# Optimization experiments

Measured on AMD Instinct MI355X. Metric: run time of the kernel, lower is better.

The kernel has to match this reference:

```python
import jax, jax.numpy as jnp
import numpy as np

EPSILON = 1e-06
MAXIMUM_AREA_RATIO = 0.3
GRID_HEIGHT = 160.0
CUBE = (25.0, 25.0, 32.0)
FEAT_SCALE = 1.0
GRID_SCALE = 1.0
CRANGE = (-1.0, 0.95)


def setup_inputs() -> dict:
    key = jax.random.key(0)
    k1, k2, k3, k4, k5 = jax.random.split(key, 5)
    B, C, H, W = 2, 256, 96, 320
    L, Wg = 128, 128
    n_layers = int(GRID_HEIGHT // CUBE[2])  # 5
    return {
        "feature": jax.random.normal(k1, (B, C, H, W), dtype=jnp.float32),
        "calib": jax.random.normal(k2, (B, 3, 4), dtype=jnp.float32),
        "grid": jax.random.normal(k3, (L, Wg, 3), dtype=jnp.float32),
        "Wc": jax.random.normal(k4, (C, C * n_layers), dtype=jnp.float32) * 0.02,
        "bc": jax.random.normal(k5, (C,), dtype=jnp.float32) * 0.02,
    }


def _cube_corners(cube):
    l, w, h = cube
    x = np.array([-l / 2, l / 2, l / 2, -l / 2, -l / 2, l / 2, l / 2, -l / 2])
    y = np.array([-w / 2, -w / 2, w / 2, w / 2, -w / 2, -w / 2, w / 2, w / 2])
    z = np.array([0, 0, 0, 0, h, h, h, h])
    return jnp.asarray(np.stack([x, y, z], axis=-1), dtype=jnp.float32)  # (8,3)


def _grid_sample_zeros(img, grd):
    # img: [B,C,H,W]; grd: [B,Hg,Wg,2] normalized coords in [-1,1]
    # bilinear, zero padding, align_corners=False (torch default)
    B, C, H, W = img.shape
    x = ((grd[..., 0] + 1.0) * W - 1.0) * 0.5
    y = ((grd[..., 1] + 1.0) * H - 1.0) * 0.5
    x0f = jnp.floor(x)
    y0f = jnp.floor(y)
    x0 = x0f.astype(jnp.int32)
    y0 = y0f.astype(jnp.int32)
    img_flat = img.reshape(B, C, H * W)

    def gather(xi, yi):
        valid = (xi >= 0) & (xi < W) & (yi >= 0) & (yi < H)
        xc = jnp.clip(xi, 0, W - 1)
        yc = jnp.clip(yi, 0, H - 1)
        idx = (yc * W + xc).reshape(B, 1, -1)
        v = jnp.take_along_axis(img_flat, idx, axis=2)
        v = v.reshape((B, C) + grd.shape[1:-1])
        return v * valid[:, None].astype(img.dtype)

    wx1 = x - x0f
    wx0 = 1.0 - wx1
    wy1 = y - y0f
    wy0 = 1.0 - wy1
    out = (gather(x0, y0) * (wx0 * wy0)[:, None]
           + gather(x0 + 1, y0) * (wx1 * wy0)[:, None]
           + gather(x0, y0 + 1) * (wx0 * wy1)[:, None]
           + gather(x0 + 1, y0 + 1) * (wx1 * wy1)[:, None])
    return out


def reference(feature, calib, grid, Wc, bc):
    B, C, H, W = feature.shape
    L, Wg, _ = grid.shape
    dtype = feature.dtype

    # z-layer offsets: (n_layers, 3) with offset only in z
    z_off = jnp.arange(0.0, GRID_HEIGHT, CUBE[2], dtype=dtype)  # (5,)
    n_layers = z_off.shape[0]
    z_corners = jnp.stack([jnp.zeros_like(z_off), jnp.zeros_like(z_off), z_off], axis=-1)
    offset = _cube_corners(CUBE)  # (8,3)

    # corners3d: (n_layers, L, Wg, 8, 3)
    corners = grid[None] + z_corners[:, None, None, :]  # (n,L,Wg,3)
    corners3d = (corners[:, :, :, None, :] + offset[None, None, None]) / GRID_SCALE

    # project with calib (B,3,4): homogeneous matmul then perspective divide
    hom = jnp.concatenate([corners3d, jnp.ones_like(corners3d[..., :1])], axis=-1)  # (n,L,Wg,8,4)
    pts = jnp.einsum('bij,nlwkj->bnlwki', calib, hom)  # (B,n,L,Wg,8,3)
    img_xy = pts[..., :2] / jnp.maximum(pts[..., 2:3], EPSILON)

    img_size = jnp.array([W, H], dtype=dtype) / FEAT_SCALE
    norm = jnp.clip(2.0 * img_xy / img_size - 1.0, CRANGE[0], CRANGE[1])  # (B,n,L,Wg,8,2)

    box_corners = jnp.concatenate([
        jnp.min(norm[..., 0], axis=-1, keepdims=True),
        jnp.min(norm[..., 1], axis=-1, keepdims=True),
        jnp.max(norm[..., 0], axis=-1, keepdims=True),
        jnp.max(norm[..., 1], axis=-1, keepdims=True),
    ], axis=-1)  # (B,n,L,Wg,4)
    box_corners = box_corners.reshape(B, n_layers, L * Wg, 4)

    area = ((box_corners[..., 2:] - box_corners[..., :2]).prod(axis=-1) * (H * W) + EPSILON)
    area = area[:, None]  # (B,1,n,LWg)
    visible = ((area > EPSILON) & (area < H * W * MAXIMUM_AREA_RATIO)).astype(dtype)

    integral = jnp.cumsum(jnp.cumsum(feature, axis=-1), axis=-2)

    lt = _grid_sample_zeros(integral, box_corners[..., [0, 1]])
    rb = _grid_sample_zeros(integral, box_corners[..., [2, 3]])
    rt = _grid_sample_zeros(integral, box_corners[..., [2, 1]])
    lb = _grid_sample_zeros(integral, box_corners[..., [0, 3]])

    vox = (lt + rb - rt - lb) / area * visible  # (B,C,n,LWg)
    # permute(0,3,1,2) -> (B, LWg, C, n); flatten to (B*LWg, C*n)
    vox = jnp.transpose(vox, (0, 3, 1, 2)).reshape(B * L * Wg, C * n_layers)

    ortho = vox @ Wc.T + bc  # (B*LWg, C)
    ortho = ortho.reshape(B, L, Wg, C)
    ortho = jax.nn.relu(jnp.transpose(ortho, (0, 3, 1, 2)))  # (B,C,L,Wg)
    return ortho
```

## Files before the change

kernel.cpp:

```cpp
#include <hip/hip_runtime.h>
#include <hip/hip_bf16.h>
#include <stdint.h>

#define BB 2
#define CC 256
#define HH 96
#define WW 320
#define NPIX 16384
#define NLAY 5
#define KDIM 1280
#define NDIM 32768
#define NKT (KDIM / 32)
#define NGRP 256

typedef float f32x4 __attribute__((ext_vector_type(4)));
typedef float f32x2 __attribute__((ext_vector_type(2)));
typedef __bf16 bf16x8 __attribute__((ext_vector_type(8)));
typedef __bf16 bf16x4 __attribute__((ext_vector_type(4)));


__global__ __launch_bounds__(1024) void k1f(const float* __restrict__ feat,
                                            float* __restrict__ integ,
                                            const float* __restrict__ gridp,
                                            const float* __restrict__ calib,
                                            const float* __restrict__ Wc,
                                            float4* __restrict__ coords,
                                            float* __restrict__ scales,
                                            __bf16* __restrict__ Wbf,
                                            uint8_t* __restrict__ mask8) {
  const int bid = blockIdx.x;
  if (bid < 480) {
    const int vbid = bid * 4 + (threadIdx.x >> 8);
    const int vt = threadIdx.x & 255;
    if (vbid >= 640) {
      int o = (vbid - 640) * 256 + vt;
      int co = o / KDIM;
      int kk = o % KDIM;
      int n = kk >> 8;
      int c = kk & 255;
      Wbf[o] = (__bf16)Wc[co * KDIM + c * NLAY + n];
      return;
    }
    int box = vbid * 256 + vt;
    int pix = box & (NPIX - 1);
    int bn = box >> 14;
    int n = bn % NLAY;
    int b = bn / NLAY;
    const float* cb = calib + b * 12;
    float c00 = cb[0], c01 = cb[1], c02 = cb[2], c03 = cb[3];
    float c10 = cb[4], c11 = cb[5], c12 = cb[6], c13 = cb[7];
    float c20 = cb[8], c21 = cb[9], c22 = cb[10], c23 = cb[11];
    float gx = gridp[pix * 3 + 0], gy = gridp[pix * 3 + 1], gz = gridp[pix * 3 + 2];
    float zoff = 32.0f * (float)n;
    const float ox[8] = {-12.5f, 12.5f, 12.5f, -12.5f, -12.5f, 12.5f, 12.5f, -12.5f};
    const float oy[8] = {-12.5f, -12.5f, 12.5f, 12.5f, -12.5f, -12.5f, 12.5f, 12.5f};
    float xmn = 1e30f, ymn = 1e30f, xmx = -1e30f, ymx = -1e30f;
#pragma unroll
    for (int k = 0; k < 8; ++k) {
      float X = gx + ox[k];
      float Y = gy + oy[k];
      float Z = gz + zoff + ((k >= 4) ? 32.0f : 0.0f);
      float px = c00 * X + c01 * Y + c02 * Z + c03;
      float py = c10 * X + c11 * Y + c12 * Z + c13;
      float pz = c20 * X + c21 * Y + c22 * Z + c23;
      float d = fmaxf(pz, 1e-6f);
      float nx = fminf(fmaxf(2.0f * (px / d) / 320.0f - 1.0f, -1.0f), 0.95f);
      float ny = fminf(fmaxf(2.0f * (py / d) / 96.0f - 1.0f, -1.0f), 0.95f);
      xmn = fminf(xmn, nx); xmx = fmaxf(xmx, nx);
      ymn = fminf(ymn, ny); ymx = fmaxf(ymx, ny);
    }
    float dx = xmx - xmn, dy = ymx - ymn;
    float area = (dx * dy) * 30720.0f + 1e-6f;
    bool vis = (area > 1e-6f) && (area < 9216.0f);
    {
      __shared__ uint32_t kf[16];
      unsigned long long bal = __ballot(vis);
      if ((threadIdx.x & 63) == 0) kf[threadIdx.x >> 6] = (bal != 0ull) ? 1u : 0u;
      __syncthreads();
      if (vt == 0) {
        int vb = threadIdx.x >> 8;
        int vbid2 = bid * 4 + vb;
        int bn2 = vbid2 >> 6;
        int n2 = bn2 % NLAY, b2 = bn2 / NLAY;
        int g0 = b2 * 128 + (vbid2 & 63) * 2;
        mask8[g0 * 5 + n2]       = (uint8_t)(kf[vb * 4 + 0] | kf[vb * 4 + 1]);
        mask8[(g0 + 1) * 5 + n2] = (uint8_t)(kf[vb * 4 + 2] | kf[vb * 4 + 3]);
      }
    }
    float X0 = ((xmn + 1.0f) * 320.0f - 1.0f) * 0.5f;
    float Y0 = ((ymn + 1.0f) * 96.0f - 1.0f) * 0.5f;
    float X1 = ((xmx + 1.0f) * 320.0f - 1.0f) * 0.5f;
    float Y1 = ((ymx + 1.0f) * 96.0f - 1.0f) * 0.5f;
    coords[box] = make_float4(X0, Y0, X1, Y1);
    scales[box] = vis ? 1.0f / area : 0.0f;
    return;
  }
  __shared__ float tile[WW * 33];
  const int t = threadIdx.x;
  const int wave = t >> 6;
  const int lane = t & 63;
  const int kb = bid - 480;
  const int cg = kb & 7;
  const int h = (kb >> 3) % HH;
  const int b = kb / (8 * HH);
  const int c0 = cg * 32 + wave * 2;
  const float* s0 = feat + (size_t)((b * CC + c0) * HH + h) * WW;
  const float* s1 = s0 + (size_t)HH * WW;

  float va[5], vb[5];
#pragma unroll
  for (int j = 0; j < 5; ++j) va[j] = s0[lane * 5 + j];
#pragma unroll
  for (int j = 0; j < 5; ++j) vb[j] = s1[lane * 5 + j];
#pragma unroll
  for (int j = 1; j < 5; ++j) { va[j] += va[j - 1]; vb[j] += vb[j - 1]; }
  float ta = va[4], tb = vb[4];
  float ia = ta, ib = tb;
#pragma unroll
  for (int d = 1; d < 64; d <<= 1) {
    float ua = __shfl_up(ia, d, 64);
    float ub = __shfl_up(ib, d, 64);
    if (lane >= d) { ia += ua; ib += ub; }
  }
  float pa = ia - ta, pb = ib - tb;
#pragma unroll
  for (int j = 0; j < 5; ++j) { va[j] += pa; vb[j] += pb; }
  const int ca = wave * 2, cbn = wave * 2 + 1;
#pragma unroll
  for (int j = 0; j < 5; ++j) {
    int w = lane * 5 + j;
    tile[w * 33 + ca]  = va[j];
    tile[w * 33 + cbn] = vb[j];
  }
  __syncthreads();
  float* dst = integ + ((size_t)(b * WW) * HH + h) * CC + cg * 32;
  const size_t wstride = (size_t)HH * CC;
#pragma unroll
  for (int r = 0; r < 3; ++r) {
    int idx = r * 1024 + t;
    if (idx < 2560) {
      int w = idx >> 3;
      int cq = (idx & 7) * 4;
      float4 o = make_float4(tile[w * 33 + cq + 0], tile[w * 33 + cq + 1],
                             tile[w * 33 + cq + 2], tile[w * 33 + cq + 3]);
      *(float4*)(dst + (size_t)w * wstride + cq) = o;
    }
  }
}

__global__ __launch_bounds__(256) void k2_scan(float* __restrict__ integ) {
  const int blk = blockIdx.x;
  const int w = blk % WW;
  const int b = blk / WW;
  const int g = threadIdx.x >> 6;
  const int l = threadIdx.x & 63;
  float* base = integ + ((size_t)(b * WW + w) * HH + g * 24) * CC + l * 4;
  const size_t stride = (size_t)CC;
  f32x4 v[24];
#pragma unroll
  for (int i = 0; i < 24; ++i) v[i] = *(const f32x4*)(base + (size_t)i * stride);
#pragma unroll
  for (int i = 1; i < 24; ++i) v[i] += v[i - 1];
  __shared__ f32x4 part[4][64];
  part[g][l] = v[23];
  __syncthreads();
  f32x4 off = {0.f, 0.f, 0.f, 0.f};
#pragma unroll
  for (int gg = 0; gg < 3; ++gg)
    if (gg < g) off += part[gg][l];
#pragma unroll
  for (int i = 0; i < 24; ++i) *(f32x4*)(base + (size_t)i * stride) = v[i] + off;
}

__global__ __launch_bounds__(256) void k4_vox(const float* __restrict__ integ,
                                              const float4* __restrict__ coords,
                                              const float* __restrict__ scales,
                                              __bf16* __restrict__ voxA,
                                              const uint8_t* __restrict__ mask8) {
  const int wave = threadIdx.x >> 6;
  const int lane = threadIdx.x & 63;
  const int box0 = (blockIdx.x * 4 + wave) * 4;
  {
    const int pix0 = box0 & (NPIX - 1);
    const int bn0 = box0 >> 14;
    const int n0 = bn0 % NLAY, b0 = bn0 / NLAY;
    if (mask8[((b0 * NPIX + pix0) >> 7) * 5 + n0] == 0) return;
  }
#pragma unroll
  for (int u = 0; u < 4; ++u) {
    const int box = box0 + u;
    const int pix = box & (NPIX - 1);
    const int bn = box >> 14;
    const int n = bn % NLAY;
    const int b = bn / NLAY;
    const size_t row = (size_t)(b * NPIX + pix);
    bf16x4* dst = (bf16x4*)(voxA + row * KDIM + n * CC + lane * 4);
    const float scale = scales[box];
    if (scale == 0.f) {
      *dst = bf16x4{(__bf16)0.f, (__bf16)0.f, (__bf16)0.f, (__bf16)0.f};
      continue;
    }
    const float4 q = coords[box];

    float xw[4]; int xi[4];
    float yw[4]; int yi[4];
    {
      float f0 = floorf(q.x); int i0 = (int)f0; float w1 = q.x - f0;
      xw[0] = (i0 >= 0 && i0 < WW) ? (1.f - w1) : 0.f;
      xw[1] = (i0 + 1 < WW) ? w1 : 0.f;
      xi[0] = min(max(i0, 0), WW - 1); xi[1] = min(max(i0 + 1, 0), WW - 1);
      float f1 = floorf(q.z); int i1 = (int)f1; float v1 = q.z - f1;
      xw[2] = (i1 >= 0 && i1 < WW) ? -(1.f - v1) : 0.f;
      xw[3] = (i1 + 1 < WW) ? -v1 : 0.f;
      xi[2] = min(max(i1, 0), WW - 1); xi[3] = min(max(i1 + 1, 0), WW - 1);
    }
    {
      float f0 = floorf(q.y); int j0 = (int)f0; float w1 = q.y - f0;
      yw[0] = (j0 >= 0 && j0 < HH) ? (1.f - w1) : 0.f;
      yw[1] = (j0 + 1 < HH) ? w1 : 0.f;
      yi[0] = min(max(j0, 0), HH - 1); yi[1] = min(max(j0 + 1, 0), HH - 1);
      float f1 = floorf(q.w); int j1 = (int)f1; float v1 = q.w - f1;
      yw[2] = (j1 >= 0 && j1 < HH) ? -(1.f - v1) : 0.f;
      yw[3] = (j1 + 1 < HH) ? -v1 : 0.f;
      yi[2] = min(max(j1, 0), HH - 1); yi[3] = min(max(j1 + 1, 0), HH - 1);
    }
    const float* base = integ + (size_t)(b * WW) * HH * CC + lane * 4;
    f32x4 val = {0.f, 0.f, 0.f, 0.f};
#pragma unroll
    for (int jj = 0; jj < 4; ++jj) {
      if (yw[jj] == 0.f) continue;
      const float* rp = base + (size_t)yi[jj] * CC;
      f32x4 rs = {0.f, 0.f, 0.f, 0.f};
#pragma unroll
      for (int ii = 0; ii < 4; ++ii) {
        if (xw[ii] != 0.f) {
          f32x4 v = *(const f32x4*)(rp + (size_t)xi[ii] * HH * CC);
          rs += xw[ii] * v;
        }
      }
      val += yw[jj] * rs;
    }
    val *= scale;
    *dst = bf16x4{(__bf16)val.x, (__bf16)val.y, (__bf16)val.z, (__bf16)val.w};
  }
}

__device__ __forceinline__ void glds16(const void* g, void* l) {
  __builtin_amdgcn_global_load_lds(
      (const __attribute__((address_space(1))) void*)g,
      (__attribute__((address_space(3))) void*)(uint32_t)(uintptr_t)l,
      16, 0, 0);
}

__global__ __launch_bounds__(256) void k6_gemm(const __bf16* __restrict__ A,
                                               const __bf16* __restrict__ Bm,
                                               const float* __restrict__ bias,
                                               float* __restrict__ out,
                                               const uint8_t* __restrict__ mask8) {
  __shared__ __align__(16) __bf16 As[4][128 * 32];
  __shared__ __align__(16) __bf16 Bs[4][128 * 32];
  __shared__ uint8_t ktsS[NKT];
  __shared__ int LsS;
  const int tileM = blockIdx.y * 128;
  const int tileN = blockIdx.x * 128;
  const int tid = threadIdx.x;
  const int lane = tid & 63;
  const int wave = tid >> 6;
  const int wm = (wave >> 1) * 64;
  const int wn = (wave & 1) * 64;

  if (tid == 0) {
    const uint8_t* mg = mask8 + blockIdx.x * 5;
    int L = 0;
#pragma unroll
    for (int n = 0; n < NLAY; ++n)
      if (mg[n]) {
#pragma unroll
        for (int kk = 0; kk < 8; ++kk) ktsS[L++] = (uint8_t)(n * 8 + kk);
      }
    LsS = L;
  }

  f32x4 acc[4][4];
#pragma unroll
  for (int i = 0; i < 4; ++i)
#pragma unroll
    for (int j = 0; j < 4; ++j)
      acc[i][j] = f32x4{0.f, 0.f, 0.f, 0.f};

  const int r16 = lane & 15;
  const int q4 = lane >> 4;
  const int srow = (lane >> 2);
  const int sch = lane & 3;

  auto stage = [&](int buf, int kt) {
    const int k0 = kt * 32;
#pragma unroll
    for (int rr = 0; rr < 2; ++rr) {
      const int base_row = wave * 16 + rr * 64;
      const int row = base_row + srow;
      const int gch = sch ^ ((row >> 1) & 3);
      glds16(A  + (size_t)(tileM + row) * KDIM + k0 + gch * 8,
             (void*)(&As[buf][base_row * 32] + lane * 8));
      glds16(Bm + (size_t)(tileN + row) * KDIM + k0 + gch * 8,
             (void*)(&Bs[buf][base_row * 32] + lane * 8));
    }
  };

  __syncthreads();
  const int L = LsS;
#pragma unroll
  for (int s = 0; s < 3; ++s)
    if (s < L) stage(s, ktsS[s]);
  for (int i = 0; i < L; ++i) {
    const int cur = i & 3;
    const int rem = L - i;
    if (rem >= 3)      __builtin_amdgcn_s_waitcnt(0xF78);
    else if (rem == 2) __builtin_amdgcn_s_waitcnt(0xF74);
    else               __builtin_amdgcn_s_waitcnt(0xF70);
    __builtin_amdgcn_s_barrier();
    if (i + 3 < L) stage((i + 3) & 3, ktsS[i + 3]);
    bf16x8 af[4], bg[4];
#pragma unroll
    for (int ii = 0; ii < 4; ++ii) {
      int m = wm + ii * 16 + r16;
      af[ii] = *(const bf16x8*)(&As[cur][m * 32] + (q4 ^ ((m >> 1) & 3)) * 8);
    }
#pragma unroll
    for (int j = 0; j < 4; ++j) {
      int nr = wn + j * 16 + r16;
      bg[j] = *(const bf16x8*)(&Bs[cur][nr * 32] + (q4 ^ ((nr >> 1) & 3)) * 8);
    }
#pragma unroll
    for (int ii = 0; ii < 4; ++ii)
#pragma unroll
      for (int j = 0; j < 4; ++j)
        acc[ii][j] = __builtin_amdgcn_mfma_f32_16x16x32_bf16(af[ii], bg[j], acc[ii][j], 0, 0, 0);
  }

#pragma unroll
  for (int i = 0; i < 4; ++i) {
#pragma unroll
    for (int j = 0; j < 4; ++j) {
      int nn = tileN + wn + j * 16 + r16;
      int bI = nn >> 14;
      int pix = nn & (NPIX - 1);
#pragma unroll
      for (int r = 0; r < 4; ++r) {
        int co = tileM + wm + i * 16 + q4 * 4 + r;
        float v = acc[i][j][r] + bias[co];
        out[(size_t)(bI * CC + co) * NPIX + pix] = fmaxf(v, 0.f);
      }
    }
  }
}

extern "C" void kernel_launch(void* const* d_in, const int* in_sizes, int n_in,
                              void* d_out, int out_size, void* d_ws, size_t ws_size,
                              hipStream_t stream) {
  const float* feat  = (const float*)d_in[0];
  const float* calib = (const float*)d_in[1];
  const float* grid  = (const float*)d_in[2];
  const float* Wc    = (const float*)d_in[3];
  const float* bc    = (const float*)d_in[4];
  float* out = (float*)d_out;

  char* ws = (char*)d_ws;
  const size_t SZ_INTEG = (size_t)BB * HH * WW * CC * 4;
  const size_t SZ_VOX   = (size_t)NDIM * KDIM * 2;
  const size_t SZ_WBF   = (size_t)CC * KDIM * 2;
  const size_t SZ_CRD   = (size_t)BB * NLAY * NPIX * 16;
  const size_t SZ_SCL   = (size_t)BB * NLAY * NPIX * 4;
  const size_t SZ_MSK   = (size_t)NGRP * NLAY;
  if (ws_size < SZ_INTEG + SZ_VOX + SZ_WBF + SZ_CRD + SZ_SCL + SZ_MSK) return;

  float*   integ  = (float*)ws;
  __bf16*  voxA   = (__bf16*)(ws + SZ_INTEG);
  __bf16*  Wbf    = (__bf16*)(ws + SZ_INTEG + SZ_VOX);
  float4*  coords = (float4*)(ws + SZ_INTEG + SZ_VOX + SZ_WBF);
  float*   scales = (float*)(ws + SZ_INTEG + SZ_VOX + SZ_WBF + SZ_CRD);
  uint8_t* mask8  = (uint8_t*)(ws + SZ_INTEG + SZ_VOX + SZ_WBF + SZ_CRD + SZ_SCL);

  k1f<<<dim3(BB * HH * 8 + 480), dim3(1024), 0, stream>>>(
      feat, integ, grid, calib, Wc, coords, scales, Wbf, mask8);
  k2_scan<<<dim3(BB * WW), dim3(256), 0, stream>>>(integ);
  k4_vox<<<dim3(BB * NLAY * NPIX / 16), dim3(256), 0, stream>>>(integ, coords, scales, voxA, mask8);
  k6_gemm<<<dim3(NDIM / 128, 2), dim3(256), 0, stream>>>(Wbf, voxA, bc, out, mask8);
}
```

Measured before the change: 161.2 us.

## Split integral image into grouped partial column sums plus scanned group-prefix table

Replaces the full-height column scan kernel with a blocked scan: each k1 block now integrates three rows and writes local partial sums plus per-group totals. A small pt_scan kernel computes the exclusive prefix over the 32 row groups, using the output buffer as scratch. The vox gather then adds the group prefix to each corner read. This removes one full read/write pass over the integral image, at the cost of an extra gather per corner in k4_vox and reliance on k6 fully overwriting the output buffer afterwards.

```diff
diff --git a/kernel.cpp b/kernel.cpp
--- a/kernel.cpp
+++ b/kernel.cpp
@@ -12,6 +12,8 @@
 #define NDIM 32768
 #define NKT (KDIM / 32)
 #define NGRP 256
+#define HG 3
+#define NHG (HH / HG)
 
 typedef float f32x4 __attribute__((ext_vector_type(4)));
 typedef float f32x2 __attribute__((ext_vector_type(2)));
@@ -19,15 +21,16 @@
 typedef __bf16 bf16x4 __attribute__((ext_vector_type(4)));
 
 
-__global__ __launch_bounds__(1024) void k1f(const float* __restrict__ feat,
-                                            float* __restrict__ integ,
+__global__ __launch_bounds__(1024) void k12(const float* __restrict__ feat,
+                                            float* __restrict__ P,
                                             const float* __restrict__ gridp,
                                             const float* __restrict__ calib,
                                             const float* __restrict__ Wc,
                                             float4* __restrict__ coords,
                                             float* __restrict__ scales,
                                             __bf16* __restrict__ Wbf,
-                                            uint8_t* __restrict__ mask8) {
+                                            uint8_t* __restrict__ mask8,
+                                            float* __restrict__ T) {
   const int bid = blockIdx.x;
   if (bid < 480) {
     const int vbid = bid * 4 + (threadIdx.x >> 8);
@@ -101,82 +104,97 @@
   const int lane = t & 63;
   const int kb = bid - 480;
   const int cg = kb & 7;
-  const int h = (kb >> 3) % HH;
-  const int b = kb / (8 * HH);
+  const int hg = (kb >> 3) & 31;
+  const int b = kb >> 8;
+  const int h0 = hg * HG;
   const int c0 = cg * 32 + wave * 2;
-  const float* s0 = feat + (size_t)((b * CC + c0) * HH + h) * WW;
+  const float* s0 = feat + (size_t)((b * CC + c0) * HH) * WW;
   const float* s1 = s0 + (size_t)HH * WW;
-
-  float va[5], vb[5];
-#pragma unroll
-  for (int j = 0; j < 5; ++j) va[j] = s0[lane * 5 + j];
-#pragma unroll
-  for (int j = 0; j < 5; ++j) vb[j] = s1[lane * 5 + j];
-#pragma unroll
-  for (int j = 1; j < 5; ++j) { va[j] += va[j - 1]; vb[j] += vb[j - 1]; }
-  float ta = va[4], tb = vb[4];
-  float ia = ta, ib = tb;
-#pragma unroll
-  for (int d = 1; d < 64; d <<= 1) {
-    float ua = __shfl_up(ia, d, 64);
-    float ub = __shfl_up(ib, d, 64);
-    if (lane >= d) { ia += ua; ib += ub; }
-  }
-  float pa = ia - ta, pb = ib - tb;
-#pragma unroll
-  for (int j = 0; j < 5; ++j) { va[j] += pa; vb[j] += pb; }
   const int ca = wave * 2, cbn = wave * 2 + 1;
-#pragma unroll
-  for (int j = 0; j < 5; ++j) {
-    int w = lane * 5 + j;
-    tile[w * 33 + ca]  = va[j];
-    tile[w * 33 + cbn] = vb[j];
-  }
-  __syncthreads();
-  float* dst = integ + ((size_t)(b * WW) * HH + h) * CC + cg * 32;
-  const size_t wstride = (size_t)HH * CC;
-#pragma unroll
-  for (int r = 0; r < 3; ++r) {
-    int idx = r * 1024 + t;
-    if (idx < 2560) {
-      int w = idx >> 3;
-      int cq = (idx & 7) * 4;
-      float4 o = make_float4(tile[w * 33 + cq + 0], tile[w * 33 + cq + 1],
-                             tile[w * 33 + cq + 2], tile[w * 33 + cq + 3]);
-      *(float4*)(dst + (size_t)w * wstride + cq) = o;
-    }
-  }
-}
-
-__global__ __launch_bounds__(256) void k2_scan(float* __restrict__ integ) {
-  const int blk = blockIdx.x;
-  const int w = blk % WW;
-  const int b = blk / WW;
-  const int g = threadIdx.x >> 6;
-  const int l = threadIdx.x & 63;
-  float* base = integ + ((size_t)(b * WW + w) * HH + g * 24) * CC + l * 4;
-  const size_t stride = (size_t)CC;
-  f32x4 v[24];
-#pragma unroll
-  for (int i = 0; i < 24; ++i) v[i] = *(const f32x4*)(base + (size_t)i * stride);
-#pragma unroll
-  for (int i = 1; i < 24; ++i) v[i] += v[i - 1];
-  __shared__ f32x4 part[4][64];
-  part[g][l] = v[23];
-  __syncthreads();
-  f32x4 off = {0.f, 0.f, 0.f, 0.f};
-#pragma unroll
-  for (int gg = 0; gg < 3; ++gg)
-    if (gg < g) off += part[gg][l];
-#pragma unroll
-  for (int i = 0; i < 24; ++i) *(f32x4*)(base + (size_t)i * stride) = v[i] + off;
-}
-
-__global__ __launch_bounds__(256) void k4_vox(const float* __restrict__ integ,
+
+  float ra[5] = {0.f, 0.f, 0.f, 0.f, 0.f};
+  float rb[5] = {0.f, 0.f, 0.f, 0.f, 0.f};
+#pragma unroll
+  for (int hh = 0; hh < HG; ++hh) {
+    const int h = h0 + hh;
+    float va[5], vb[5];
+#pragma unroll
+    for (int j = 0; j < 5; ++j) va[j] = s0[(size_t)h * WW + lane * 5 + j];
+#pragma unroll
+    for (int j = 0; j < 5; ++j) vb[j] = s1[(size_t)h * WW + lane * 5 + j];
+#pragma unroll
+    for (int j = 1; j < 5; ++j) { va[j] += va[j - 1]; vb[j] += vb[j - 1]; }
+    float ta = va[4], tb = vb[4];
+    float ia = ta, ib = tb;
+#pragma unroll
+    for (int d = 1; d < 64; d <<= 1) {
+      float ua = __shfl_up(ia, d, 64);
+      float ub = __shfl_up(ib, d, 64);
+      if (lane >= d) { ia += ua; ib += ub; }
+    }
+    float pa = ia - ta, pb = ib - tb;
+#pragma unroll
+    for (int j = 0; j < 5; ++j) {
+      va[j] += pa; vb[j] += pb;
+      ra[j] += va[j]; rb[j] += vb[j];
+    }
+#pragma unroll
+    for (int j = 0; j < 5; ++j) {
+      int w = lane * 5 + j;
+      tile[w * 33 + ca]  = ra[j];
+      tile[w * 33 + cbn] = rb[j];
+    }
+    __syncthreads();
+    float* dst = P + ((size_t)(b * WW) * HH + h) * CC + cg * 32;
+#pragma unroll
+    for (int r = 0; r < 3; ++r) {
+      int idx = r * 1024 + t;
+      if (idx < 2560) {
+        int w = idx >> 3;
+        int cq = (idx & 7) * 4;
+        float4 o = make_float4(tile[w * 33 + cq + 0], tile[w * 33 + cq + 1],
+                               tile[w * 33 + cq + 2], tile[w * 33 + cq + 3]);
+        *(float4*)(dst + (size_t)w * HH * CC + cq) = o;
+      }
+    }
+    if (hh == HG - 1) {
+      float* td = T + ((size_t)(b * NHG + hg) * WW) * CC + cg * 32;
+#pragma unroll
+      for (int r = 0; r < 3; ++r) {
+        int idx = r * 1024 + t;
+        if (idx < 2560) {
+          int w = idx >> 3;
+          int cq = (idx & 7) * 4;
+          float4 o = make_float4(tile[w * 33 + cq + 0], tile[w * 33 + cq + 1],
+                                 tile[w * 33 + cq + 2], tile[w * 33 + cq + 3]);
+          *(float4*)(td + (size_t)w * CC + cq) = o;
+        }
+      }
+    }
+    __syncthreads();
+  }
+}
+
+__global__ __launch_bounds__(256) void pt_scan(float* __restrict__ T) {
+  const int w = blockIdx.x % WW;
+  const int b = blockIdx.x / WW;
+  const int c = threadIdx.x;
+  float* p = T + ((size_t)(b * NHG) * WW + w) * CC + c;
+  const size_t gs = (size_t)WW * CC;
+  float v[NHG];
+#pragma unroll
+  for (int g = 0; g < NHG; ++g) v[g] = p[(size_t)g * gs];
+  float run = 0.f;
+#pragma unroll
+  for (int g = 0; g < NHG; ++g) { float x = v[g]; p[(size_t)g * gs] = run; run += x; }
+}
+
+__global__ __launch_bounds__(256) void k4_vox(const float* __restrict__ P,
                                               const float4* __restrict__ coords,
                                               const float* __restrict__ scales,
                                               __bf16* __restrict__ voxA,
-                                              const uint8_t* __restrict__ mask8) {
+                                              const uint8_t* __restrict__ mask8,
+                                              const float* __restrict__ PT) {
   const int wave = threadIdx.x >> 6;
   const int lane = threadIdx.x & 63;
   const int box0 = (blockIdx.x * 4 + wave) * 4;
@@ -224,17 +242,21 @@
       yw[3] = (j1 + 1 < HH) ? -v1 : 0.f;
       yi[2] = min(max(j1, 0), HH - 1); yi[3] = min(max(j1 + 1, 0), HH - 1);
     }
-    const float* base = integ + (size_t)(b * WW) * HH * CC + lane * 4;
+    const float* base = P + (size_t)(b * WW) * HH * CC + lane * 4;
+    const float* ptb = PT + (size_t)(b * NHG) * WW * CC + lane * 4;
     f32x4 val = {0.f, 0.f, 0.f, 0.f};
 #pragma unroll
     for (int jj = 0; jj < 4; ++jj) {
       if (yw[jj] == 0.f) continue;
+      const int yg = yi[jj] / HG;
       const float* rp = base + (size_t)yi[jj] * CC;
+      const float* pp = ptb + (size_t)yg * WW * CC;
       f32x4 rs = {0.f, 0.f, 0.f, 0.f};
 #pragma unroll
       for (int ii = 0; ii < 4; ++ii) {
         if (xw[ii] != 0.f) {
-          f32x4 v = *(const f32x4*)(rp + (size_t)xi[ii] * HH * CC);
+          f32x4 v = *(const f32x4*)(rp + (size_t)xi[ii] * HH * CC)
+                  + *(const f32x4*)(pp + (size_t)xi[ii] * CC);
           rs += xw[ii] * v;
         }
       }
@@ -372,7 +394,9 @@
   const size_t SZ_CRD   = (size_t)BB * NLAY * NPIX * 16;
   const size_t SZ_SCL   = (size_t)BB * NLAY * NPIX * 4;
   const size_t SZ_MSK   = (size_t)NGRP * NLAY;
+  const size_t NT_ELEM  = (size_t)BB * NHG * WW * CC;
   if (ws_size < SZ_INTEG + SZ_VOX + SZ_WBF + SZ_CRD + SZ_SCL + SZ_MSK) return;
+  if ((size_t)out_size < NT_ELEM) return;
 
   float*   integ  = (float*)ws;
   __bf16*  voxA   = (__bf16*)(ws + SZ_INTEG);
@@ -380,10 +404,12 @@
   float4*  coords = (float4*)(ws + SZ_INTEG + SZ_VOX + SZ_WBF);
   float*   scales = (float*)(ws + SZ_INTEG + SZ_VOX + SZ_WBF + SZ_CRD);
   uint8_t* mask8  = (uint8_t*)(ws + SZ_INTEG + SZ_VOX + SZ_WBF + SZ_CRD + SZ_SCL);
-
-  k1f<<<dim3(BB * HH * 8 + 480), dim3(1024), 0, stream>>>(
-      feat, integ, grid, calib, Wc, coords, scales, Wbf, mask8);
-  k2_scan<<<dim3(BB * WW), dim3(256), 0, stream>>>(integ);
-  k4_vox<<<dim3(BB * NLAY * NPIX / 16), dim3(256), 0, stream>>>(integ, coords, scales, voxA, mask8);
+  float*   Tscr   = out;
+
+  k12<<<dim3(480 + BB * NHG * 8), dim3(1024), 0, stream>>>(
+      feat, integ, grid, calib, Wc, coords, scales, Wbf, mask8, Tscr);
+  pt_scan<<<dim3(BB * WW), dim3(256), 0, stream>>>(Tscr);
+  k4_vox<<<dim3(BB * NLAY * NPIX / 16), dim3(256), 0, stream>>>(
+      integ, coords, scales, voxA, mask8, Tscr);
   k6_gemm<<<dim3(NDIM / 128, 2), dim3(256), 0, stream>>>(Wbf, voxA, bc, out, mask8);
 }
```

After: 155.4 us. 3.6% less time.
